# Kernel tuning notes

Measured on AMD Instinct MI355X. Metric: run time of the kernel, lower is better.

The kernel has to match this reference:

```python
import jax, jax.numpy as jnp
import numpy as np

H = 16
D_IN = 1024
D_OUT = 1024
D_K = D_OUT // H
B = 8
S = 1024


def setup_inputs() -> dict:
    key = jax.random.key(0)
    ks = jax.random.split(key, 9)
    scale = 1.0 / np.sqrt(D_IN)
    inp = {
        "query": jax.random.normal(ks[0], (B, S, D_IN), dtype=jnp.float32),
        "key_": jax.random.normal(ks[1], (B, S, D_IN), dtype=jnp.float32),
        "value": jax.random.normal(ks[2], (B, S, D_IN), dtype=jnp.float32),
        "Wq": jax.random.uniform(ks[3], (D_OUT, D_IN), jnp.float32, -scale, scale),
        "bq": jax.random.uniform(ks[4], (D_OUT,), jnp.float32, -scale, scale),
        "Wk": jax.random.uniform(ks[5], (D_OUT, D_IN), jnp.float32, -scale, scale),
        "bk": jax.random.uniform(ks[6], (D_OUT,), jnp.float32, -scale, scale),
        "Wv": jax.random.uniform(ks[7], (D_OUT, D_IN), jnp.float32, -scale, scale),
        "bv": jax.random.uniform(ks[8], (D_OUT,), jnp.float32, -scale, scale),
    }
    return inp


def reference(query, key_, value, Wq, bq, Wk, bk, Wv, bv):
    batch = query.shape[0]

    def proj(x, W, b):
        # torch Linear: x @ W.T + b, then view(B, -1, h, d_k).transpose(1, 2)
        y = jnp.einsum("bsd,od->bso", x, W) + b
        return y.reshape(batch, -1, H, D_K).transpose(0, 2, 1, 3)  # [B, h, S, d_k]

    q = proj(query, Wq, bq)
    k = proj(key_, Wk, bk)
    v = proj(value, Wv, bv)

    scores = jnp.einsum("bhqd,bhkd->bhqk", q, k) / (D_K ** 0.5)  # [B, h, S, S]
    attn = jax.nn.softmax(scores, axis=-1)
    x = jnp.einsum("bhqk,bhkd->bhqd", attn, v)  # [B, h, S, d_k]

    # transpose(1, 2).contiguous().view(batch, -1) -> flatten seq*d_out
    return x.transpose(0, 2, 1, 3).reshape(batch, -1)
```

## Files before the change

### kernel.cpp

```cpp
#include <hip/hip_runtime.h>
#include <math.h>

#define NH   16
#define DK   64
#define SEQL 1024
#define NB   8
#define DIN  1024

typedef __bf16 bf16;
typedef __attribute__((ext_vector_type(8))) __bf16 bf16x8;
typedef __attribute__((ext_vector_type(4))) __bf16 bf16x4;
typedef __attribute__((ext_vector_type(4))) float f32x4;

#define QSCALE 0.18033688011112042f

static __device__ __forceinline__ f32x4 mfma_bf16(bf16x8 a, bf16x8 b, f32x4 c) {
  return __builtin_amdgcn_mfma_f32_16x16x32_bf16(a, b, c, 0, 0, 0);
}

static __device__ __forceinline__ void async16(const bf16* g, bf16* l) {
  __builtin_amdgcn_global_load_lds(
      (const __attribute__((address_space(1))) void*)g,
      (__attribute__((address_space(3))) void*)l, 16, 0, 0);
}

__global__ __launch_bounds__(256)
void cvt_kernel(const float* __restrict__ s, bf16* __restrict__ d, int n8) {
  const int i = blockIdx.x * 256 + threadIdx.x;
  if (i >= n8) return;
  const f32x4* sp = (const f32x4*)s;
  const f32x4 a = sp[2 * i], b = sp[2 * i + 1];
  bf16x8 r;
  r[0] = (bf16)a[0]; r[1] = (bf16)a[1]; r[2] = (bf16)a[2]; r[3] = (bf16)a[3];
  r[4] = (bf16)b[0]; r[5] = (bf16)b[1]; r[6] = (bf16)b[2]; r[7] = (bf16)b[3];
  ((bf16x8*)d)[i] = r;
}

__global__ __launch_bounds__(256, 2)
void proj_kernel(const bf16* __restrict__ X, const bf16* __restrict__ W,
                 const float* __restrict__ Bi, bf16* __restrict__ Y,
                 int zmode) {
  const int m0 = blockIdx.x * 128;
  const int n0 = blockIdx.y * 128;

  __shared__ __attribute__((aligned(16))) bf16 As[128 * 32];
  __shared__ __attribute__((aligned(16))) bf16 Bs[128 * 32];

  const int t    = threadIdx.x;
  const int l    = t & 63;
  const int w    = t >> 6;
  const int l15  = l & 15;
  const int quad = l >> 4;
  const int wm   = w & 1;
  const int wn   = w >> 1;

  f32x4 acc[4][4];
#pragma unroll
  for (int i = 0; i < 4; ++i)
#pragma unroll
    for (int j = 0; j < 4; ++j) acc[i][j] = (f32x4){0.f, 0.f, 0.f, 0.f};

  const int srow   = l >> 2;
  const int gchunk = (l & 3) ^ ((l >> 3) & 3);

  for (int k0 = 0; k0 < DIN; k0 += 32) {
    __syncthreads();
#pragma unroll
    for (int i = 0; i < 2; ++i) {
      const int slab = w * 32 + i * 16;
      const int r    = slab + srow;
      async16(X + (size_t)(m0 + r) * DIN + k0 + gchunk * 8, As + slab * 32);
      async16(W + (size_t)(n0 + r) * DIN + k0 + gchunk * 8, Bs + slab * 32);
    }
    __syncthreads();

    bf16x8 af[4], bfr[4];
    const int swz = quad ^ ((l15 >> 1) & 3);
#pragma unroll
    for (int mi = 0; mi < 4; ++mi)
      af[mi] = *(const bf16x8*)(As + (wm * 64 + mi * 16 + l15) * 32 + swz * 8);
#pragma unroll
    for (int nj = 0; nj < 4; ++nj)
      bfr[nj] = *(const bf16x8*)(Bs + (wn * 64 + nj * 16 + l15) * 32 + swz * 8);
#pragma unroll
    for (int mi = 0; mi < 4; ++mi)
#pragma unroll
      for (int nj = 0; nj < 4; ++nj)
        acc[mi][nj] = mfma_bf16(af[mi], bfr[nj], acc[mi][nj]);
  }

  if (zmode == 2) {
#pragma unroll
    for (int nj = 0; nj < 4; ++nj) {
      const int o    = n0 + wn * 64 + nj * 16 + l15;
      const float bv = Bi[o];
      const int h    = o >> 6;
      const int d    = o & 63;
#pragma unroll
      for (int mi = 0; mi < 4; ++mi) {
        const int m  = m0 + wm * 64 + mi * 16 + quad * 4;
        const int bl = m >> 10;
        const int s  = m & (SEQL - 1);
        bf16x4 pk;
#pragma unroll
        for (int r = 0; r < 4; ++r) pk[r] = (bf16)(acc[mi][nj][r] + bv);
        *(bf16x4*)(Y + ((size_t)(bl * NH + h) * DK + d) * SEQL + s) = pk;
      }
    }
  } else {
    const float scale = (zmode == 0) ? QSCALE : 1.0f;
#pragma unroll
    for (int nj = 0; nj < 4; ++nj) {
      const int o    = n0 + wn * 64 + nj * 16 + l15;
      const float bv = Bi[o];
      const int h    = o >> 6;
      const int d    = o & 63;
#pragma unroll
      for (int mi = 0; mi < 4; ++mi) {
#pragma unroll
        for (int r = 0; r < 4; ++r) {
          const int m  = m0 + wm * 64 + mi * 16 + quad * 4 + r;
          const int bl = m >> 10;
          const int s  = m & (SEQL - 1);
          Y[(size_t)(((bl * NH + h) << 10) | s) * DK + d] =
              (bf16)((acc[mi][nj][r] + bv) * scale);
        }
      }
    }
  }
}

__global__ __launch_bounds__(256, 2)
void attn_kernel(const bf16* __restrict__ Q, const bf16* __restrict__ K,
                 const bf16* __restrict__ V, float* __restrict__ Out, int b0) {
  const int bhl = blockIdx.x;
  const int q0  = blockIdx.y * 128;
  const int bg  = b0 + (bhl >> 4);
  const int h   = bhl & 15;
  const int t    = threadIdx.x;
  const int l    = t & 63;
  const int w    = t >> 6;
  const int l15  = l & 15;
  const int quad = l >> 4;

  const bf16* Qh = Q + (size_t)bhl * SEQL * DK;
  const bf16* Kh = K + (size_t)bhl * SEQL * DK;
  const bf16* Vh = V + (size_t)bhl * DK * SEQL;

  __shared__ __attribute__((aligned(16))) bf16 sKs[32 * 64];
  __shared__ __attribute__((aligned(16))) bf16 sVt[64 * 32];
  __shared__ __attribute__((aligned(16))) bf16 sPl[4][2][640];

  bf16x8 qf[2][2];
#pragma unroll
  for (int g = 0; g < 2; ++g)
#pragma unroll
    for (int hh = 0; hh < 2; ++hh)
      qf[g][hh] = *(const bf16x8*)(Qh + (size_t)(q0 + w * 32 + g * 16 + l15) * DK +
                                   hh * 32 + quad * 8);

  bf16x8 ones;
#pragma unroll
  for (int j = 0; j < 8; ++j) ones[j] = (bf16)1.0f;

  f32x4 oacc[2][4];
#pragma unroll
  for (int g = 0; g < 2; ++g)
#pragma unroll
    for (int n = 0; n < 4; ++n) oacc[g][n] = (f32x4){0.f, 0.f, 0.f, 0.f};
  f32x4 sacc[2];
  sacc[0] = (f32x4){0.f, 0.f, 0.f, 0.f};
  sacc[1] = (f32x4){0.f, 0.f, 0.f, 0.f};

  for (int kb = 0; kb < SEQL; kb += 32) {
    __syncthreads();
    async16(Kh + (size_t)(kb + w * 8 + (l >> 3)) * DK +
                ((l & 7) ^ ((l >> 3) & 7)) * 8,
            sKs + w * 8 * 64);
    async16(Vh + (size_t)(w * 16 + (l >> 2)) * SEQL + kb +
                ((l & 3) ^ ((l >> 3) & 3)) * 8,
            sVt + w * 16 * 32);
    __syncthreads();

    bf16x8 kf[2][2];
#pragma unroll
    for (int ss = 0; ss < 2; ++ss)
#pragma unroll
      for (int hh = 0; hh < 2; ++hh)
        kf[ss][hh] = *(const bf16x8*)(sKs + (ss * 16 + l15) * 64 +
                                      (((hh * 4 + quad) ^ (l15 & 7)) * 8));

#pragma unroll
    for (int g = 0; g < 2; ++g) {
      f32x4 cs0 = (f32x4){0.f, 0.f, 0.f, 0.f};
      f32x4 cs1 = (f32x4){0.f, 0.f, 0.f, 0.f};
      cs0 = mfma_bf16(qf[g][0], kf[0][0], cs0);
      cs0 = mfma_bf16(qf[g][1], kf[0][1], cs0);
      cs1 = mfma_bf16(qf[g][0], kf[1][0], cs1);
      cs1 = mfma_bf16(qf[g][1], kf[1][1], cs1);
#pragma unroll
      for (int r = 0; r < 4; ++r) {
        sPl[w][g][(quad * 4 + r) * 40 + l15]      = (bf16)exp2f(cs0[r]);
        sPl[w][g][(quad * 4 + r) * 40 + 16 + l15] = (bf16)exp2f(cs1[r]);
      }
    }
    __syncthreads();

    bf16x8 vfr[4];
#pragma unroll
    for (int n = 0; n < 4; ++n)
      vfr[n] = *(const bf16x8*)(sVt + (n * 16 + l15) * 32 +
                                ((quad ^ ((l15 >> 1) & 3)) * 8));
#pragma unroll
    for (int g = 0; g < 2; ++g) {
      const bf16x8 pf = *(const bf16x8*)(&sPl[w][g][l15 * 40 + quad * 8]);
#pragma unroll
      for (int n = 0; n < 4; ++n)
        oacc[g][n] = mfma_bf16(pf, vfr[n], oacc[g][n]);
      sacc[g] = mfma_bf16(pf, ones, sacc[g]);
    }
  }

#pragma unroll
  for (int g = 0; g < 2; ++g) {
    float linv[4];
#pragma unroll
    for (int r = 0; r < 4; ++r) linv[r] = 1.0f / sacc[g][r];
#pragma unroll
    for (int n = 0; n < 4; ++n) {
      const int d = n * 16 + l15;
#pragma unroll
      for (int r = 0; r < 4; ++r) {
        const int qrow = q0 + w * 32 + g * 16 + quad * 4 + r;
        Out[(size_t)((bg * SEQL + qrow) * NH + h) * DK + d] =
            oacc[g][n][r] * linv[r];
      }
    }
  }
}

extern "C" void kernel_launch(void* const* d_in, const int* in_sizes, int n_in,
                              void* d_out, int out_size, void* d_ws,
                              size_t ws_size, hipStream_t stream) {
  const float* q  = (const float*)d_in[0];
  const float* k  = (const float*)d_in[1];
  const float* v  = (const float*)d_in[2];
  const float* Wq = (const float*)d_in[3];
  const float* bq = (const float*)d_in[4];
  const float* Wk = (const float*)d_in[5];
  const float* bk = (const float*)d_in[6];
  const float* Wv = (const float*)d_in[7];
  const float* bv = (const float*)d_in[8];
  float* out = (float*)d_out;

  const size_t wElems = (size_t)DIN * DIN;
  const size_t wBytes = 3 * wElems * sizeof(bf16);
  const size_t perBatch = 6 * (size_t)SEQL * DIN * sizeof(bf16);
  int nbg = (ws_size > wBytes) ? (int)((ws_size - wBytes) / perBatch) : 1;
  if (nbg < 1) nbg = 1;
  if (nbg > NB) nbg = NB;

  bf16* Wqb = (bf16*)d_ws;
  bf16* Wkb = Wqb + wElems;
  bf16* Wvb = Wkb + wElems;
  const size_t g1 = (size_t)nbg * SEQL * DIN;
  bf16* Xqb = Wvb + wElems;
  bf16* Xkb = Xqb + g1;
  bf16* Xvb = Xkb + g1;
  bf16* Yqb = Xvb + g1;
  bf16* Ykb = Yqb + g1;
  bf16* Yvb = Ykb + g1;

  const int w8 = (int)(wElems / 8);
  cvt_kernel<<<(w8 + 255) / 256, 256, 0, stream>>>(Wq, Wqb, w8);
  cvt_kernel<<<(w8 + 255) / 256, 256, 0, stream>>>(Wk, Wkb, w8);
  cvt_kernel<<<(w8 + 255) / 256, 256, 0, stream>>>(Wv, Wvb, w8);

  for (int b0 = 0; b0 < NB; b0 += nbg) {
    const int nb = (NB - b0 < nbg) ? (NB - b0) : nbg;
    const int n8 = nb * SEQL * DIN / 8;
    const size_t xoff = (size_t)b0 * SEQL * DIN;
    cvt_kernel<<<(n8 + 255) / 256, 256, 0, stream>>>(q + xoff, Xqb, n8);
    cvt_kernel<<<(n8 + 255) / 256, 256, 0, stream>>>(k + xoff, Xkb, n8);
    cvt_kernel<<<(n8 + 255) / 256, 256, 0, stream>>>(v + xoff, Xvb, n8);

    dim3 gP(nb * 8, 8);
    proj_kernel<<<gP, 256, 0, stream>>>(Xqb, Wqb, bq, Yqb, 0);
    proj_kernel<<<gP, 256, 0, stream>>>(Xkb, Wkb, bk, Ykb, 1);
    proj_kernel<<<gP, 256, 0, stream>>>(Xvb, Wvb, bv, Yvb, 2);

    dim3 gA(nb * NH, SEQL / 128);
    attn_kernel<<<gA, 256, 0, stream>>>(Yqb, Ykb, Yvb, out, b0);
  }
}
```

Before: 299.7 us.

## Batch Q/K/V conversions and projections into single launches and widen attention key tile

The three fp32-to-bf16 conversion launches and the three projection launches are each merged into one grid using a z/y dimension to pick the Q, K or V operands. This cuts launch count and lets the three independent workloads share the GPU at once. The attention kernel now processes 64 keys per iteration instead of 32. It computes S^T via swapped MFMA operands so P is written in vectorized bf16x4 stores, and drops one __syncthreads per iteration since each wave reads only its own P slice. The tradeoff is more LDS per block and more live registers in attention.

```diff
diff --git a/kernel.cpp b/kernel.cpp
--- a/kernel.cpp
+++ b/kernel.cpp
@@ -25,9 +25,13 @@
 }
 
 __global__ __launch_bounds__(256)
-void cvt_kernel(const float* __restrict__ s, bf16* __restrict__ d, int n8) {
+void cvt3_kernel(const float* __restrict__ s0, const float* __restrict__ s1,
+                 const float* __restrict__ s2, bf16* __restrict__ d0,
+                 bf16* __restrict__ d1, bf16* __restrict__ d2, int n8) {
   const int i = blockIdx.x * 256 + threadIdx.x;
   if (i >= n8) return;
+  const float* s = (blockIdx.y == 0) ? s0 : (blockIdx.y == 1) ? s1 : s2;
+  bf16*        d = (blockIdx.y == 0) ? d0 : (blockIdx.y == 1) ? d1 : d2;
   const f32x4* sp = (const f32x4*)s;
   const f32x4 a = sp[2 * i], b = sp[2 * i + 1];
   bf16x8 r;
@@ -37,9 +41,20 @@
 }
 
 __global__ __launch_bounds__(256, 2)
-void proj_kernel(const bf16* __restrict__ X, const bf16* __restrict__ W,
-                 const float* __restrict__ Bi, bf16* __restrict__ Y,
-                 int zmode) {
+void proj_kernel(const bf16* __restrict__ Xq, const bf16* __restrict__ Xk,
+                 const bf16* __restrict__ Xv,
+                 const bf16* __restrict__ Wq, const bf16* __restrict__ Wk,
+                 const bf16* __restrict__ Wv,
+                 const float* __restrict__ Bq, const float* __restrict__ Bk,
+                 const float* __restrict__ Bv,
+                 bf16* __restrict__ Yq, bf16* __restrict__ Yk,
+                 bf16* __restrict__ Yv) {
+  const int z = blockIdx.z;
+  const bf16*  X  = (z == 0) ? Xq : (z == 1) ? Xk : Xv;
+  const bf16*  W  = (z == 0) ? Wq : (z == 1) ? Wk : Wv;
+  const float* Bi = (z == 0) ? Bq : (z == 1) ? Bk : Bv;
+  bf16*        Y  = (z == 0) ? Yq : (z == 1) ? Yk : Yv;
+
   const int m0 = blockIdx.x * 128;
   const int n0 = blockIdx.y * 128;
 
@@ -89,7 +104,7 @@
         acc[mi][nj] = mfma_bf16(af[mi], bfr[nj], acc[mi][nj]);
   }
 
-  if (zmode == 2) {
+  if (z == 2) {
 #pragma unroll
     for (int nj = 0; nj < 4; ++nj) {
       const int o    = n0 + wn * 64 + nj * 16 + l15;
@@ -108,7 +123,7 @@
       }
     }
   } else {
-    const float scale = (zmode == 0) ? QSCALE : 1.0f;
+    const float scale = (z == 0) ? QSCALE : 1.0f;
 #pragma unroll
     for (int nj = 0; nj < 4; ++nj) {
       const int o    = n0 + wn * 64 + nj * 16 + l15;
@@ -147,9 +162,9 @@
   const bf16* Kh = K + (size_t)bhl * SEQL * DK;
   const bf16* Vh = V + (size_t)bhl * DK * SEQL;
 
-  __shared__ __attribute__((aligned(16))) bf16 sKs[32 * 64];
-  __shared__ __attribute__((aligned(16))) bf16 sVt[64 * 32];
-  __shared__ __attribute__((aligned(16))) bf16 sPl[4][2][640];
+  __shared__ __attribute__((aligned(16))) bf16 sKs[64 * 64];
+  __shared__ __attribute__((aligned(16))) bf16 sVt[64 * 64];
+  __shared__ __attribute__((aligned(16))) bf16 sPl[4][2][16 * 72];
 
   bf16x8 qf[2][2];
 #pragma unroll
@@ -172,52 +187,61 @@
   sacc[0] = (f32x4){0.f, 0.f, 0.f, 0.f};
   sacc[1] = (f32x4){0.f, 0.f, 0.f, 0.f};
 
-  for (int kb = 0; kb < SEQL; kb += 32) {
+  const int drow   = l >> 3;
+  const int dchunk = l & 7;
+
+  for (int kb = 0; kb < SEQL; kb += 64) {
     __syncthreads();
-    async16(Kh + (size_t)(kb + w * 8 + (l >> 3)) * DK +
-                ((l & 7) ^ ((l >> 3) & 7)) * 8,
-            sKs + w * 8 * 64);
-    async16(Vh + (size_t)(w * 16 + (l >> 2)) * SEQL + kb +
-                ((l & 3) ^ ((l >> 3) & 3)) * 8,
-            sVt + w * 16 * 32);
+#pragma unroll
+    for (int i = 0; i < 2; ++i) {
+      const int r = w * 16 + i * 8 + drow;
+      async16(Kh + (size_t)(kb + r) * DK + (dchunk ^ (r & 7)) * 8,
+              sKs + (w * 16 + i * 8) * 64);
+      async16(Vh + (size_t)r * SEQL + kb + (dchunk ^ (r & 7)) * 8,
+              sVt + (w * 16 + i * 8) * 64);
+    }
     __syncthreads();
 
-    bf16x8 kf[2][2];
-#pragma unroll
-    for (int ss = 0; ss < 2; ++ss)
+    bf16x8 kf[4][2];
+#pragma unroll
+    for (int c = 0; c < 4; ++c)
 #pragma unroll
       for (int hh = 0; hh < 2; ++hh)
-        kf[ss][hh] = *(const bf16x8*)(sKs + (ss * 16 + l15) * 64 +
+        kf[c][hh] = *(const bf16x8*)(sKs + (c * 16 + l15) * 64 +
+                                     (((hh * 4 + quad) ^ (l15 & 7)) * 8));
+
+#pragma unroll
+    for (int g = 0; g < 2; ++g) {
+#pragma unroll
+      for (int c = 0; c < 4; ++c) {
+        f32x4 cs = (f32x4){0.f, 0.f, 0.f, 0.f};
+        cs = mfma_bf16(kf[c][0], qf[g][0], cs);
+        cs = mfma_bf16(kf[c][1], qf[g][1], cs);
+        bf16x4 pk;
+#pragma unroll
+        for (int r = 0; r < 4; ++r) pk[r] = (bf16)exp2f(cs[r]);
+        *(bf16x4*)(&sPl[w][g][l15 * 72 + c * 16 + quad * 4]) = pk;
+      }
+    }
+
+    bf16x8 vfr[4][2];
+#pragma unroll
+    for (int n = 0; n < 4; ++n)
+#pragma unroll
+      for (int hh = 0; hh < 2; ++hh)
+        vfr[n][hh] = *(const bf16x8*)(sVt + (n * 16 + l15) * 64 +
                                       (((hh * 4 + quad) ^ (l15 & 7)) * 8));
-
 #pragma unroll
     for (int g = 0; g < 2; ++g) {
-      f32x4 cs0 = (f32x4){0.f, 0.f, 0.f, 0.f};
-      f32x4 cs1 = (f32x4){0.f, 0.f, 0.f, 0.f};
-      cs0 = mfma_bf16(qf[g][0], kf[0][0], cs0);
-      cs0 = mfma_bf16(qf[g][1], kf[0][1], cs0);
-      cs1 = mfma_bf16(qf[g][0], kf[1][0], cs1);
-      cs1 = mfma_bf16(qf[g][1], kf[1][1], cs1);
-#pragma unroll
-      for (int r = 0; r < 4; ++r) {
-        sPl[w][g][(quad * 4 + r) * 40 + l15]      = (bf16)exp2f(cs0[r]);
-        sPl[w][g][(quad * 4 + r) * 40 + 16 + l15] = (bf16)exp2f(cs1[r]);
-      }
-    }
-    __syncthreads();
-
-    bf16x8 vfr[4];
-#pragma unroll
-    for (int n = 0; n < 4; ++n)
-      vfr[n] = *(const bf16x8*)(sVt + (n * 16 + l15) * 32 +
-                                ((quad ^ ((l15 >> 1) & 3)) * 8));
-#pragma unroll
-    for (int g = 0; g < 2; ++g) {
-      const bf16x8 pf = *(const bf16x8*)(&sPl[w][g][l15 * 40 + quad * 8]);
-#pragma unroll
-      for (int n = 0; n < 4; ++n)
-        oacc[g][n] = mfma_bf16(pf, vfr[n], oacc[g][n]);
-      sacc[g] = mfma_bf16(pf, ones, sacc[g]);
+      const bf16x8 pf0 = *(const bf16x8*)(&sPl[w][g][l15 * 72 + quad * 8]);
+      const bf16x8 pf1 = *(const bf16x8*)(&sPl[w][g][l15 * 72 + 32 + quad * 8]);
+#pragma unroll
+      for (int n = 0; n < 4; ++n) {
+        oacc[g][n] = mfma_bf16(pf0, vfr[n][0], oacc[g][n]);
+        oacc[g][n] = mfma_bf16(pf1, vfr[n][1], oacc[g][n]);
+      }
+      sacc[g] = mfma_bf16(pf0, ones, sacc[g]);
+      sacc[g] = mfma_bf16(pf1, ones, sacc[g]);
     }
   }
 
@@ -272,22 +296,20 @@
   bf16* Yvb = Ykb + g1;
 
   const int w8 = (int)(wElems / 8);
-  cvt_kernel<<<(w8 + 255) / 256, 256, 0, stream>>>(Wq, Wqb, w8);
-  cvt_kernel<<<(w8 + 255) / 256, 256, 0, stream>>>(Wk, Wkb, w8);
-  cvt_kernel<<<(w8 + 255) / 256, 256, 0, stream>>>(Wv, Wvb, w8);
+  dim3 gW((w8 + 255) / 256, 3);
+  cvt3_kernel<<<gW, 256, 0, stream>>>(Wq, Wk, Wv, Wqb, Wkb, Wvb, w8);
 
   for (int b0 = 0; b0 < NB; b0 += nbg) {
     const int nb = (NB - b0 < nbg) ? (NB - b0) : nbg;
     const int n8 = nb * SEQL * DIN / 8;
     const size_t xoff = (size_t)b0 * SEQL * DIN;
-    cvt_kernel<<<(n8 + 255) / 256, 256, 0, stream>>>(q + xoff, Xqb, n8);
-    cvt_kernel<<<(n8 + 255) / 256, 256, 0, stream>>>(k + xoff, Xkb, n8);
-    cvt_kernel<<<(n8 + 255) / 256, 256, 0, stream>>>(v + xoff, Xvb, n8);
-
-    dim3 gP(nb * 8, 8);
-    proj_kernel<<<gP, 256, 0, stream>>>(Xqb, Wqb, bq, Yqb, 0);
-    proj_kernel<<<gP, 256, 0, stream>>>(Xkb, Wkb, bk, Ykb, 1);
-    proj_kernel<<<gP, 256, 0, stream>>>(Xvb, Wvb, bv, Yvb, 2);
+    dim3 gX((n8 + 255) / 256, 3);
+    cvt3_kernel<<<gX, 256, 0, stream>>>(q + xoff, k + xoff, v + xoff,
+                                        Xqb, Xkb, Xvb, n8);
+
+    dim3 gP(nb * 8, 8, 3);
+    proj_kernel<<<gP, 256, 0, stream>>>(Xqb, Xkb, Xvb, Wqb, Wkb, Wvb,
+                                        bq, bk, bv, Yqb, Ykb, Yvb);
 
     dim3 gA(nb * NH, SEQL / 128);
     attn_kernel<<<gA, 256, 0, stream>>>(Yqb, Ykb, Yvb, out, b0);
```

Measured after the change: 282.0 us. -5.9%, faster.
